# Kernel tuning notes

Hardware: AMD Instinct MI355X
Metric: run time of the kernel (lower is better)

The kernel has to match this reference:

```python
import jax, jax.numpy as jnp
import numpy as np

TOP_K = 8


def setup_inputs() -> dict:
    key = jax.random.key(0)
    ks = jax.random.split(key, 5)
    T, H, I, E = 4096, 2048, 1024, 64
    s = 0.02
    return {
        "x": jax.random.normal(ks[0], (T, H), jnp.float32),
        "gate_w": jax.random.normal(ks[1], (E, H), jnp.float32) * s,
        "gate_b": jax.random.normal(ks[2], (E,), jnp.float32) * s,
        "fc1_w": jax.random.normal(ks[3], (E, 2 * I, H), jnp.float32) * s,
        "fc2_w": jax.random.normal(ks[4], (E, H, I), jnp.float32) * s,
    }


def reference(x, gate_w, gate_b, fc1_w, fc2_w):
    # Router: [T, E] logits, top-k, softmax over selected logits in fp32.
    E = gate_w.shape[0]
    logits = x @ gate_w.T + gate_b
    topk_logits, topk_idx = jax.lax.top_k(logits, TOP_K)
    w = jax.nn.softmax(topk_logits.astype(jnp.float32), axis=-1).astype(x.dtype)
    # Per-token combine weight for each expert: [T, E] (0 if expert not selected).
    comb = (jax.nn.one_hot(topk_idx, E, dtype=x.dtype) * w[..., None]).sum(axis=1)
    # Scan over experts: each step is one dense GEMM-GeGLU-GEMM with masked combine.
    def body(acc, ew):
        W1, W2, c = ew  # W1 [2I, H], W2 [H, I], c [T]
        h_full = x @ W1.T                       # [T, 2I]
        h, g = jnp.split(h_full, 2, axis=-1)
        a = jax.nn.gelu(h, approximate=False) * (g + 1.0)  # custom GeGLU
        y = a @ W2.T                            # [T, H]
        return acc + c[:, None] * y, None

    out0 = jnp.zeros_like(x)
    out, _ = jax.lax.scan(body, out0, (fc1_w, fc2_w, comb.T))
    return out
```

## Files before the change

kernel.cpp:

```cpp
#include <hip/hip_runtime.h>
#include <hip/hip_bf16.h>
#include <cfloat>
#include <math.h>

#define T_TOK 4096
#define H_DIM 2048
#define E_NUM 64
#define I_DIM 1024
#define TOPK  8
#define BM    256
#define BK    64
#define MAXT  192

typedef __attribute__((ext_vector_type(4))) float f32x4;
typedef __attribute__((ext_vector_type(8))) short bf16x8;
typedef __attribute__((ext_vector_type(4))) int   i32x4;

__device__ __forceinline__ unsigned short f2bf(float f) {
    union { float f; unsigned int u; } v; v.f = f;
    unsigned int r = v.u + 0x7FFFu + ((v.u >> 16) & 1u);
    return (unsigned short)(r >> 16);
}
__device__ __forceinline__ unsigned int pack2(float a, float b) {
    return (unsigned int)f2bf(a) | ((unsigned int)f2bf(b) << 16);
}
__device__ __forceinline__ float bf2f(unsigned short u) {
    union { unsigned int u; float f; } v; v.u = (unsigned int)u << 16; return v.f;
}
__device__ __forceinline__ int cvtpk(float lo, float hi) {
    int r; asm("v_cvt_pk_bf16_f32 %0, %1, %2" : "=v"(r) : "v"(lo), "v"(hi)); return r;
}
__device__ __forceinline__ void gload16(const void* g, void* l) {
    __builtin_amdgcn_global_load_lds((const __attribute__((address_space(1))) unsigned int*)g,
                                     (__attribute__((address_space(3))) unsigned int*)l, 16, 0, 0);
}

__global__ __launch_bounds__(256)
void router_kernel(const float* __restrict__ x, const float* __restrict__ gw,
                   const float* __restrict__ gb, unsigned short* __restrict__ xb,
                   int* __restrict__ topk_idx, float* __restrict__ topk_w,
                   int* __restrict__ counts)
{
    const int t = blockIdx.x;
    const int tid = threadIdx.x;
    __shared__ float xs[H_DIM];
    __shared__ float logits[E_NUM];
    const float* xrow = x + (size_t)t * H_DIM;

    #pragma unroll
    for (int i = 0; i < 2; ++i) {
        int c = i * 1024 + tid * 4;
        f32x4 v = *(const f32x4*)(xrow + c);
        *(f32x4*)(xs + c) = v;
        uint2 pk; pk.x = pack2(v.x, v.y); pk.y = pack2(v.z, v.w);
        *(uint2*)(xb + (size_t)t * H_DIM + c) = pk;
    }
    __syncthreads();

    const int wave = tid >> 6, lane = tid & 63;
    for (int ee = 0; ee < 16; ++ee) {
        const int e = wave * 16 + ee;
        const float* g = gw + (size_t)e * H_DIM;
        float p = 0.f;
        #pragma unroll
        for (int i = 0; i < 8; ++i) {
            int c = (i * 64 + lane) * 4;
            f32x4 gv = *(const f32x4*)(g + c);
            f32x4 xv = *(const f32x4*)(xs + c);
            p += gv.x * xv.x + gv.y * xv.y + gv.z * xv.z + gv.w * xv.w;
        }
        #pragma unroll
        for (int s = 32; s > 0; s >>= 1) p += __shfl_xor(p, s, 64);
        if (lane == 0) logits[e] = p + gb[e];
    }
    __syncthreads();

    if (tid < 64) {
        float cur = logits[tid];
        float wv[TOPK]; int wi[TOPK];
        #pragma unroll
        for (int k = 0; k < TOPK; ++k) {
            float bv = cur; int bi = tid;
            #pragma unroll
            for (int s = 32; s > 0; s >>= 1) {
                float ov = __shfl_xor(bv, s, 64);
                int   oi = __shfl_xor(bi, s, 64);
                if (ov > bv || (ov == bv && oi < bi)) { bv = ov; bi = oi; }
            }
            wv[k] = bv; wi[k] = bi;
            if (tid == bi) cur = -FLT_MAX;
        }
        if (tid == 0) {
            float mx = wv[0], sum = 0.f, ex[TOPK];
            #pragma unroll
            for (int k = 0; k < TOPK; ++k) { ex[k] = expf(wv[k] - mx); sum += ex[k]; }
            #pragma unroll
            for (int k = 0; k < TOPK; ++k) {
                topk_idx[t * TOPK + k] = wi[k];
                topk_w[t * TOPK + k]   = ex[k] / sum;
                atomicAdd(&counts[wi[k]], 1);
            }
        }
    }
}

__global__ void scan_kernel(const int* __restrict__ counts, int* __restrict__ offsets,
                            int* __restrict__ cursors, int* __restrict__ tiles,
                            int* __restrict__ ntiles)
{
    if (threadIdx.x == 0) {
        int acc = 0, nt = 0;
        for (int e = 0; e < E_NUM; ++e) {
            offsets[e] = acc; cursors[e] = acc;
            int c = counts[e];
            for (int m = 0; m * BM < c; ++m) tiles[nt++] = (e << 16) | m;
            acc += c;
        }
        *ntiles = nt;
    }
}

__global__ void assign_kernel(const int* __restrict__ topk_idx, const float* __restrict__ topk_w,
                              int* __restrict__ cursors, int* __restrict__ tok_of,
                              int* __restrict__ pos_of)
{
    int i = blockIdx.x * 256 + threadIdx.x;
    if (i >= T_TOK * TOPK) return;
    int e = topk_idx[i];
    int pos = atomicAdd(&cursors[e], 1);
    tok_of[pos] = i >> 3;
    pos_of[i]   = pos;
}

__global__ __launch_bounds__(512, 1)
void gemm1_kernel(const unsigned short* __restrict__ xb, const float* __restrict__ fc1,
                  const int* __restrict__ counts, const int* __restrict__ offsets,
                  const int* __restrict__ tok_of, const int* __restrict__ tiles,
                  const int* __restrict__ ntiles, unsigned short* __restrict__ a_all)
{
    const int ty = blockIdx.y;
    if (ty >= *ntiles) return;
    const int code = tiles[ty];
    const int e = code >> 16, m0 = (code & 0xffff) * BM;
    const int cnt = counts[e], off = offsets[e];
    const int pn0 = blockIdx.x * 128;
    const float* W = fc1 + (size_t)e * (size_t)(2 * I_DIM) * H_DIM;

    __shared__ unsigned short sA[2][BM * BK];
    __shared__ unsigned short sB[2][BM * BK];
    __shared__ int sTok[BM];

    const int tid = threadIdx.x;
    if (tid < BM) {
        int m = m0 + tid;
        sTok[tid] = tok_of[off + (m < cnt ? m : cnt - 1)];
    }
    __syncthreads();

    const int wid = tid >> 6, lane = tid & 63;
    const int srow = tid >> 3, sch = tid & 7;
    const int brow = tid >> 1, bhalf = tid & 1;

    const unsigned short* aSrc[4];
    #pragma unroll
    for (int i = 0; i < 4; ++i) {
        int row = srow + 64 * i;
        aSrc[i] = xb + (size_t)sTok[row] * H_DIM + (sch ^ (row & 7)) * 8;
    }
    const int wrow = (brow < 128) ? (pn0 + brow) : (I_DIM + pn0 + (brow - 128));
    const float* bSrc = W + (size_t)wrow * H_DIM + bhalf * 32;

    f32x4 accH[8][2], accG[8][2];
    #pragma unroll
    for (int m = 0; m < 8; ++m)
        #pragma unroll
        for (int n = 0; n < 2; ++n) {
            accH[m][n] = (f32x4){0.f, 0.f, 0.f, 0.f};
            accG[m][n] = (f32x4){0.f, 0.f, 0.f, 0.f};
        }

    const int wm = (wid >> 2) * 128;
    const int wn = (wid & 3) * 32;
    const int fr = lane & 15;
    const int kg = lane >> 4;

    f32x4 br[8];

    auto issueB = [&](int k0) {
        #pragma unroll
        for (int j = 0; j < 8; ++j) br[j] = *(const f32x4*)(bSrc + k0 + j * 4);
    };
    auto issueA = [&](int k0, int buf) {
        #pragma unroll
        for (int i = 0; i < 4; ++i)
            gload16(aSrc[i] + k0, &sA[buf][i * 4096 + tid * 8]);
    };
    auto writeB = [&](int buf) {
        #pragma unroll
        for (int j = 0; j < 4; ++j) {
            i32x4 pk = (i32x4){cvtpk(br[2*j].x,   br[2*j].y),
                               cvtpk(br[2*j].z,   br[2*j].w),
                               cvtpk(br[2*j+1].x, br[2*j+1].y),
                               cvtpk(br[2*j+1].z, br[2*j+1].w)};
            int s = bhalf * 4 + j;
            *(i32x4*)((char*)sB[buf] + brow * 128 + ((s ^ (brow & 7)) * 16)) = pk;
        }
    };
    auto compute = [&](int buf) {
        #pragma unroll
        for (int kk = 0; kk < 2; ++kk) {
            bf16x8 af[8], bh[2], bg[2];
            #pragma unroll
            for (int m = 0; m < 8; ++m) {
                int row = wm + m * 16 + fr;
                af[m] = *(const bf16x8*)((const char*)sA[buf] +
                        row * 128 + (((kk * 4 + kg) ^ (row & 7)) * 16));
            }
            #pragma unroll
            for (int n = 0; n < 2; ++n) {
                int rh = wn + n * 16 + fr;
                bh[n] = *(const bf16x8*)((const char*)sB[buf] +
                        rh * 128 + (((kk * 4 + kg) ^ (rh & 7)) * 16));
                int rg = 128 + rh;
                bg[n] = *(const bf16x8*)((const char*)sB[buf] +
                        rg * 128 + (((kk * 4 + kg) ^ (rg & 7)) * 16));
            }
            __builtin_amdgcn_s_setprio(1);
            #pragma unroll
            for (int m = 0; m < 8; ++m)
                #pragma unroll
                for (int n = 0; n < 2; ++n) {
                    accH[m][n] = __builtin_amdgcn_mfma_f32_16x16x32_bf16(af[m], bh[n], accH[m][n], 0, 0, 0);
                    accG[m][n] = __builtin_amdgcn_mfma_f32_16x16x32_bf16(af[m], bg[n], accG[m][n], 0, 0, 0);
                }
            __builtin_amdgcn_s_setprio(0);
        }
    };

    const int NT = H_DIM / BK;
    issueB(0);
    issueA(0, 0);
    __syncthreads();
    writeB(0);
    __syncthreads();
    int cur = 0;
    for (int t = 0; t < NT; ++t) {
        const bool more = (t + 1) < NT;
        if (more) { issueB((t + 1) * BK); issueA((t + 1) * BK, cur ^ 1); }
        compute(cur);
        __syncthreads();
        if (more) writeB(cur ^ 1);
        __syncthreads();
        cur ^= 1;
    }

    #pragma unroll
    for (int m = 0; m < 8; ++m) {
        int rbase = wm + m * 16 + kg * 4;
        #pragma unroll
        for (int r = 0; r < 4; ++r) {
            int gm = m0 + rbase + r;
            if (gm < cnt) {
                size_t rowoff = (size_t)(off + gm) * I_DIM + pn0 + wn;
                #pragma unroll
                for (int n = 0; n < 2; ++n) {
                    float h = accH[m][n][r];
                    float g = accG[m][n][r];
                    float a = 0.5f * h * (1.f + erff(h * 0.70710678118f)) * (g + 1.f);
                    a_all[rowoff + n * 16 + fr] = f2bf(a);
                }
            }
        }
    }
}

__global__ __launch_bounds__(512, 1)
void gemm2_kernel(const unsigned short* __restrict__ a_all, const float* __restrict__ fc2,
                  const int* __restrict__ counts, const int* __restrict__ offsets,
                  const int* __restrict__ tiles, const int* __restrict__ ntiles,
                  unsigned short* __restrict__ y)
{
    const int ty = blockIdx.y;
    if (ty >= *ntiles) return;
    const int code = tiles[ty];
    const int e = code >> 16, m0 = (code & 0xffff) * BM;
    const int cnt = counts[e], off = offsets[e];
    const int n0 = blockIdx.x * 256;
    const float* W = fc2 + (size_t)e * (size_t)H_DIM * I_DIM;

    __shared__ unsigned short sA[2][BM * BK];
    __shared__ unsigned short sB[2][BM * BK];

    const int tid = threadIdx.x;
    const int wid = tid >> 6, lane = tid & 63;
    const int srow = tid >> 3, sch = tid & 7;
    const int brow = tid >> 1, bhalf = tid & 1;

    const unsigned short* aSrc[4];
    #pragma unroll
    for (int i = 0; i < 4; ++i) {
        int row = srow + 64 * i;
        aSrc[i] = a_all + (size_t)(off + m0 + row) * I_DIM + (sch ^ (row & 7)) * 8;
    }
    const float* bSrc = W + (size_t)(n0 + brow) * I_DIM + bhalf * 32;

    f32x4 acc[8][4];
    #pragma unroll
    for (int m = 0; m < 8; ++m)
        #pragma unroll
        for (int n = 0; n < 4; ++n) acc[m][n] = (f32x4){0.f, 0.f, 0.f, 0.f};

    const int wm = (wid >> 2) * 128;
    const int wn = (wid & 3) * 64;
    const int fr = lane & 15;
    const int kg = lane >> 4;

    f32x4 br[8];

    auto issueB = [&](int k0) {
        #pragma unroll
        for (int j = 0; j < 8; ++j) br[j] = *(const f32x4*)(bSrc + k0 + j * 4);
    };
    auto issueA = [&](int k0, int buf) {
        #pragma unroll
        for (int i = 0; i < 4; ++i)
            gload16(aSrc[i] + k0, &sA[buf][i * 4096 + tid * 8]);
    };
    auto writeB = [&](int buf) {
        #pragma unroll
        for (int j = 0; j < 4; ++j) {
            i32x4 pk = (i32x4){cvtpk(br[2*j].x,   br[2*j].y),
                               cvtpk(br[2*j].z,   br[2*j].w),
                               cvtpk(br[2*j+1].x, br[2*j+1].y),
                               cvtpk(br[2*j+1].z, br[2*j+1].w)};
            int s = bhalf * 4 + j;
            *(i32x4*)((char*)sB[buf] + brow * 128 + ((s ^ (brow & 7)) * 16)) = pk;
        }
    };
    auto compute = [&](int buf) {
        #pragma unroll
        for (int kk = 0; kk < 2; ++kk) {
            bf16x8 af[8], bf[4];
            #pragma unroll
            for (int m = 0; m < 8; ++m) {
                int row = wm + m * 16 + fr;
                af[m] = *(const bf16x8*)((const char*)sA[buf] +
                        row * 128 + (((kk * 4 + kg) ^ (row & 7)) * 16));
            }
            #pragma unroll
            for (int n = 0; n < 4; ++n) {
                int row = wn + n * 16 + fr;
                bf[n] = *(const bf16x8*)((const char*)sB[buf] +
                        row * 128 + (((kk * 4 + kg) ^ (row & 7)) * 16));
            }
            __builtin_amdgcn_s_setprio(1);
            #pragma unroll
            for (int m = 0; m < 8; ++m)
                #pragma unroll
                for (int n = 0; n < 4; ++n)
                    acc[m][n] = __builtin_amdgcn_mfma_f32_16x16x32_bf16(af[m], bf[n], acc[m][n], 0, 0, 0);
            __builtin_amdgcn_s_setprio(0);
        }
    };

    const int NT = I_DIM / BK;
    issueB(0);
    issueA(0, 0);
    __syncthreads();
    writeB(0);
    __syncthreads();
    int cur = 0;
    for (int t = 0; t < NT; ++t) {
        const bool more = (t + 1) < NT;
        if (more) { issueB((t + 1) * BK); issueA((t + 1) * BK, cur ^ 1); }
        compute(cur);
        __syncthreads();
        if (more) writeB(cur ^ 1);
        __syncthreads();
        cur ^= 1;
    }

    #pragma unroll
    for (int m = 0; m < 8; ++m) {
        int rbase = wm + m * 16 + kg * 4;
        #pragma unroll
        for (int r = 0; r < 4; ++r) {
            int gm = m0 + rbase + r;
            if (gm < cnt) {
                size_t rowoff = (size_t)(off + gm) * H_DIM + n0 + wn;
                #pragma unroll
                for (int n = 0; n < 4; ++n)
                    y[rowoff + n * 16 + fr] = f2bf(acc[m][n][r]);
            }
        }
    }
}

__global__ __launch_bounds__(256)
void combine_kernel(const unsigned short* __restrict__ y, const int* __restrict__ pos_of,
                    const float* __restrict__ topk_w, float* __restrict__ out)
{
    const int t = blockIdx.x;
    const int tid = threadIdx.x;
    __shared__ int   sp[TOPK];
    __shared__ float sw[TOPK];
    if (tid < TOPK) {
        sp[tid] = pos_of[t * TOPK + tid];
        sw[tid] = topk_w[t * TOPK + tid];
    }
    __syncthreads();

    const int c0 = tid * 8;
    float acc[8];
    #pragma unroll
    for (int j = 0; j < 8; ++j) acc[j] = 0.f;
    #pragma unroll
    for (int k = 0; k < TOPK; ++k) {
        const float w = sw[k];
        i32x4 v = *(const i32x4*)(y + (size_t)sp[k] * H_DIM + c0);
        const unsigned short* u = (const unsigned short*)&v;
        #pragma unroll
        for (int j = 0; j < 8; ++j) acc[j] += w * bf2f(u[j]);
    }
    float* orow = out + (size_t)t * H_DIM + c0;
    *(f32x4*)orow       = (f32x4){acc[0], acc[1], acc[2], acc[3]};
    *(f32x4*)(orow + 4) = (f32x4){acc[4], acc[5], acc[6], acc[7]};
}

extern "C" void kernel_launch(void* const* d_in, const int* in_sizes, int n_in,
                              void* d_out, int out_size, void* d_ws, size_t ws_size,
                              hipStream_t stream)
{
    const float* x   = (const float*)d_in[0];
    const float* gw  = (const float*)d_in[1];
    const float* gb  = (const float*)d_in[2];
    const float* fc1 = (const float*)d_in[3];
    const float* fc2 = (const float*)d_in[4];
    float* out = (float*)d_out;

    char* ws = (char*)d_ws;
    size_t o = 0;
    auto alloc = [&](size_t b) { void* p = ws + o; o = (o + b + 255) & ~(size_t)255; return p; };
    unsigned short* xb     = (unsigned short*)alloc((size_t)T_TOK * H_DIM * 2);
    int*            tk_idx = (int*)  alloc((size_t)T_TOK * TOPK * 4);
    float*          tk_w   = (float*)alloc((size_t)T_TOK * TOPK * 4);
    int*            counts = (int*)  alloc(E_NUM * 4);
    int*            offs   = (int*)  alloc(E_NUM * 4);
    int*            curs   = (int*)  alloc(E_NUM * 4);
    int*            tiles  = (int*)  alloc(MAXT * 4);
    int*            ntiles = (int*)  alloc(4);
    int*            tok_of = (int*)  alloc((size_t)T_TOK * TOPK * 4);
    int*            pos_of = (int*)  alloc((size_t)T_TOK * TOPK * 4);
    unsigned short* a_all  = (unsigned short*)alloc((size_t)(T_TOK * TOPK + BM) * I_DIM * 2);
    unsigned short* yb     = (unsigned short*)alloc((size_t)(T_TOK * TOPK + BM) * H_DIM * 2);
    (void)ws_size;

    hipMemsetAsync(counts, 0, E_NUM * 4, stream);

    router_kernel<<<T_TOK, 256, 0, stream>>>(x, gw, gb, xb, tk_idx, tk_w, counts);
    scan_kernel<<<1, 64, 0, stream>>>(counts, offs, curs, tiles, ntiles);
    assign_kernel<<<(T_TOK * TOPK + 255) / 256, 256, 0, stream>>>(tk_idx, tk_w, curs, tok_of, pos_of);
    gemm1_kernel<<<dim3(I_DIM / 128, MAXT), 512, 0, stream>>>(xb, fc1, counts, offs, tok_of,
                                                              tiles, ntiles, a_all);
    gemm2_kernel<<<dim3(H_DIM / 256, MAXT), 512, 0, stream>>>(a_all, fc2, counts, offs,
                                                              tiles, ntiles, yb);
    combine_kernel<<<T_TOK, 256, 0, stream>>>(yb, pos_of, tk_w, out);
}
```

Before: 1.393 ms.

## Prefetch B two tiles ahead with manual vmcnt waits and one barrier

Restructures the main loop of both expert GEMM kernels so B (fp32 weights) is loaded into registers two k-tiles ahead and converted and stored to LDS before compute of the current tile. The two __syncthreads per iteration become explicit s_waitcnt vmcnt/lgkmcnt plus a single s_barrier, and the loop is kept rolled. The aim is to hide global-load latency behind MFMA compute and cut barrier overhead. In exchange the manual vmcnt counts must match the exact number of outstanding loads, which is fragile, and the store to the other buffer now happens while other waves may still be reading it.

```diff
diff --git a/kernel.cpp b/kernel.cpp
--- a/kernel.cpp
+++ b/kernel.cpp
@@ -34,6 +34,11 @@
     __builtin_amdgcn_global_load_lds((const __attribute__((address_space(1))) unsigned int*)g,
                                      (__attribute__((address_space(3))) unsigned int*)l, 16, 0, 0);
 }
+#define WAIT_VM4   do { asm volatile("s_waitcnt vmcnt(4)" ::: "memory"); __builtin_amdgcn_sched_barrier(0); } while(0)
+#define WAIT_VM8   do { asm volatile("s_waitcnt vmcnt(8)" ::: "memory"); __builtin_amdgcn_sched_barrier(0); } while(0)
+#define WAIT_VM0   do { asm volatile("s_waitcnt vmcnt(0)" ::: "memory"); __builtin_amdgcn_sched_barrier(0); } while(0)
+#define WAIT_LGKM0 do { asm volatile("s_waitcnt lgkmcnt(0)" ::: "memory"); __builtin_amdgcn_sched_barrier(0); } while(0)
+#define BAR __builtin_amdgcn_s_barrier()
 
 __global__ __launch_bounds__(256)
 void router_kernel(const float* __restrict__ x, const float* __restrict__ gw,
@@ -186,7 +191,7 @@
 
     f32x4 br[8];
 
-    auto issueB = [&](int k0) {
+    auto loadB = [&](int k0) {
         #pragma unroll
         for (int j = 0; j < 8; ++j) br[j] = *(const f32x4*)(bSrc + k0 + j * 4);
     };
@@ -195,7 +200,7 @@
         for (int i = 0; i < 4; ++i)
             gload16(aSrc[i] + k0, &sA[buf][i * 4096 + tid * 8]);
     };
-    auto writeB = [&](int buf) {
+    auto storeB = [&](int buf) {
         #pragma unroll
         for (int j = 0; j < 4; ++j) {
             i32x4 pk = (i32x4){cvtpk(br[2*j].x,   br[2*j].y),
@@ -238,19 +243,30 @@
     };
 
     const int NT = H_DIM / BK;
-    issueB(0);
+    loadB(0);
     issueA(0, 0);
-    __syncthreads();
-    writeB(0);
-    __syncthreads();
+    WAIT_VM4;
+    storeB(0);
+    loadB(BK);
+    WAIT_VM8;
+    WAIT_LGKM0;
+    BAR;
+
     int cur = 0;
+    #pragma unroll 1
     for (int t = 0; t < NT; ++t) {
-        const bool more = (t + 1) < NT;
-        if (more) { issueB((t + 1) * BK); issueA((t + 1) * BK, cur ^ 1); }
+        const bool n1 = (t + 1) < NT, n2 = (t + 2) < NT;
+        if (n1) {
+            issueA((t + 1) * BK, cur ^ 1);
+            WAIT_VM4;
+            storeB(cur ^ 1);
+        }
+        if (n2) loadB((t + 2) * BK);
         compute(cur);
-        __syncthreads();
-        if (more) writeB(cur ^ 1);
-        __syncthreads();
+        if (n2)      { WAIT_VM8; }
+        else if (n1) { WAIT_VM0; }
+        WAIT_LGKM0;
+        BAR;
         cur ^= 1;
     }
 
@@ -317,7 +333,7 @@
 
     f32x4 br[8];
 
-    auto issueB = [&](int k0) {
+    auto loadB = [&](int k0) {
         #pragma unroll
         for (int j = 0; j < 8; ++j) br[j] = *(const f32x4*)(bSrc + k0 + j * 4);
     };
@@ -326,7 +342,7 @@
         for (int i = 0; i < 4; ++i)
             gload16(aSrc[i] + k0, &sA[buf][i * 4096 + tid * 8]);
     };
-    auto writeB = [&](int buf) {
+    auto storeB = [&](int buf) {
         #pragma unroll
         for (int j = 0; j < 4; ++j) {
             i32x4 pk = (i32x4){cvtpk(br[2*j].x,   br[2*j].y),
@@ -364,19 +380,30 @@
     };
 
     const int NT = I_DIM / BK;
-    issueB(0);
+    loadB(0);
     issueA(0, 0);
-    __syncthreads();
-    writeB(0);
-    __syncthreads();
+    WAIT_VM4;
+    storeB(0);
+    loadB(BK);
+    WAIT_VM8;
+    WAIT_LGKM0;
+    BAR;
+
     int cur = 0;
+    #pragma unroll 1
     for (int t = 0; t < NT; ++t) {
-        const bool more = (t + 1) < NT;
-        if (more) { issueB((t + 1) * BK); issueA((t + 1) * BK, cur ^ 1); }
+        const bool n1 = (t + 1) < NT, n2 = (t + 2) < NT;
+        if (n1) {
+            issueA((t + 1) * BK, cur ^ 1);
+            WAIT_VM4;
+            storeB(cur ^ 1);
+        }
+        if (n2) loadB((t + 2) * BK);
         compute(cur);
-        __syncthreads();
-        if (more) writeB(cur ^ 1);
-        __syncthreads();
+        if (n2)      { WAIT_VM8; }
+        else if (n1) { WAIT_VM0; }
+        WAIT_LGKM0;
+        BAR;
         cur ^= 1;
     }
 
```

After: 1.313 ms. -5.8%, faster.
